# Kernel tuning notes

Hardware: AMD Instinct MI355X
Metric: run time of the kernel (lower is better)

## Reference

```python
import jax, jax.numpy as jnp
import numpy as np

N_NODES = 100000
D = 128
E_ER = 800000
E_EE = 800000
E_RR = 400000


def setup_inputs() -> dict:
    key = jax.random.key(0)
    ks = jax.random.split(key, 16)
    def lin(kw, kb, out_d, in_d):
        s = 1.0 / np.sqrt(in_d)
        w = jax.random.uniform(kw, (out_d, in_d), minval=-s, maxval=s, dtype=jnp.float32)
        b = jax.random.uniform(kb, (out_d,), minval=-s, maxval=s, dtype=jnp.float32)
        return w, b
    W_attn_w, W_attn_b = lin(ks[0], ks[1], D, 2 * D)
    w0_w, w0_b = lin(ks[2], ks[3], 1, D)
    W1_w, W1_b = lin(ks[4], ks[5], D, D)
    W2_w, W2_b = lin(ks[6], ks[7], D, D)
    W3_w, W3_b = lin(ks[8], ks[9], D, D)
    return {
        "node_emb": jax.random.normal(ks[10], (N_NODES, D), dtype=jnp.float32),
        "er_src": jax.random.randint(ks[11], (E_ER,), 0, N_NODES),
        "er_dst": jax.random.randint(ks[12], (E_ER,), 0, N_NODES),
        "ee_src": jax.random.randint(ks[13], (E_EE,), 0, N_NODES),
        "ee_dst": jax.random.randint(ks[14], (E_EE,), 0, N_NODES),
        "ee_weight": jax.random.uniform(ks[15], (E_EE,), dtype=jnp.float32),
        "rr_src": jax.random.randint(jax.random.fold_in(key, 100), (E_RR,), 0, N_NODES),
        "rr_dst": jax.random.randint(jax.random.fold_in(key, 101), (E_RR,), 0, N_NODES),
        "W_attn_w": W_attn_w, "W_attn_b": W_attn_b,
        "w0_w": w0_w, "w0_b": w0_b,
        "W1_w": W1_w, "W1_b": W1_b,
        "W2_w": W2_w, "W2_b": W2_b,
        "W3_w": W3_w, "W3_b": W3_b,
    }


def _segment_softmax(values, segment_ids, num_segments):
    # torch version: seg_max initialized to zeros with include_self=True -> max(0, seg max)
    seg_max = jnp.maximum(jax.ops.segment_max(values, segment_ids, num_segments=num_segments), 0.0)
    exp_v = jnp.exp(values - seg_max[segment_ids])
    seg_sum = jax.ops.segment_sum(exp_v, segment_ids, num_segments=num_segments)
    return exp_v / (seg_sum[segment_ids] + 1e-9)


def reference(node_emb, er_src, er_dst, ee_src, ee_dst, ee_weight, rr_src, rr_dst,
              W_attn_w, W_attn_b, w0_w, w0_b, W1_w, W1_b, W2_w, W2_b, W3_w, W3_b):
    N = node_emb.shape[0]
    # --- attention aggregation over er edges (entity <- relation) ---
    h_emb = node_emb[er_src]            # (E, D)
    r_emb = node_emb[er_dst]            # (E, D)
    pair = jnp.concatenate([r_emb, h_emb], axis=-1)  # (E, 2D)
    e_ij = (jnp.tanh(pair @ W_attn_w.T + W_attn_b) @ w0_w.T + w0_b)[:, 0]  # (E,)
    attn = _segment_softmax(e_ij, er_src, N)
    attn_agg = jax.ops.segment_sum(attn[:, None] * r_emb, er_src, num_segments=N)
    # --- mean aggregation ---
    mean_agg = jax.ops.segment_sum(h_emb, er_dst, num_segments=N)
    mean_cnt = jax.ops.segment_sum(jnp.ones_like(er_dst, dtype=node_emb.dtype), er_dst, num_segments=N)
    w = ee_weight[:, None]
    mean_agg = mean_agg + jax.ops.segment_sum(w * node_emb[ee_dst], ee_src, num_segments=N)
    mean_cnt = mean_cnt + jax.ops.segment_sum(ee_weight, ee_src, num_segments=N)
    mean_agg = mean_agg + jax.ops.segment_sum(node_emb[rr_dst], rr_src, num_segments=N)
    mean_cnt = mean_cnt + jax.ops.segment_sum(jnp.ones_like(rr_src, dtype=node_emb.dtype), rr_src, num_segments=N)
    mean_agg = mean_agg / jnp.clip(mean_cnt, 1.0, None)[:, None]
    return (jnp.tanh(node_emb @ W1_w.T + W1_b)
            + jnp.tanh(attn_agg @ W2_w.T + W2_b)
            + jnp.tanh(mean_agg @ W3_w.T + W3_b))
```

## Files before the change

kernel.cpp:

```cpp
#include <hip/hip_runtime.h>

typedef unsigned int u32;
typedef unsigned short u16;

#define D 128

typedef __attribute__((ext_vector_type(8))) short bf16x8;
typedef __attribute__((ext_vector_type(4))) float f32x4;
#define MFMA16x16(a, b, c) __builtin_amdgcn_mfma_f32_16x16x32_bf16(a, b, c, 0, 0, 0)

__device__ inline float b2f(u32 h) { return __uint_as_float((h & 0xffffu) << 16); }
__device__ inline u16 f2b(float f) {
    u32 u = __float_as_uint(f);
    return (u16)((u + 0x7fffu + ((u >> 16) & 1u)) >> 16);
}
__device__ inline float tanh_fast(float x) {
    x = fminf(fmaxf(x, -15.f), 15.f);
    float e = __expf(2.f * x);
    return (e - 1.f) * __builtin_amdgcn_rcpf(e + 1.f);
}


__global__ __launch_bounds__(256) void k_bhist(const int* __restrict__ er_src,
                                               const int* __restrict__ er_dst,
                                               const int* __restrict__ ee_src,
                                               const int* __restrict__ rr_src,
                                               int* __restrict__ histA,
                                               int* __restrict__ histM,
                                               int E_ER, int E_EE, int E_RR, int NBK) {
    __shared__ int hA[1024], hM[1024];
    int tid = threadIdx.x;
    for (int j = tid; j < NBK; j += 256) { hA[j] = 0; hM[j] = 0; }
    __syncthreads();
    int E_T = 2 * E_ER + E_EE + E_RR;
    int stride = gridDim.x * 256;
    for (int e = blockIdx.x * 256 + tid; e < E_T; e += stride) {
        int i = e;
        if (i < E_ER) { atomicAdd(&hA[er_src[i] >> 7], 1); continue; }
        i -= E_ER;
        int key;
        if (i < E_ER) key = er_dst[i];
        else {
            i -= E_ER;
            key = (i < E_EE) ? ee_src[i] : rr_src[i - E_EE];
        }
        atomicAdd(&hM[key >> 7], 1);
    }
    __syncthreads();
    for (int j = tid; j < NBK; j += 256) {
        histA[j * 256 + blockIdx.x] = hA[j];
        histM[j * 256 + blockIdx.x] = hM[j];
    }
}

__global__ void k_scan1_dual(const int* __restrict__ cnt2, int n,
                             int* __restrict__ off_src, int* __restrict__ off_mean,
                             int* __restrict__ bsum, int nbs) {
    __shared__ int sh[256];
    int b = blockIdx.x;
    const int* cnt = cnt2;
    int* out = off_src;
    int* bs = bsum;
    if (b >= nbs) { b -= nbs; cnt = cnt2 + n; out = off_mean; bs = bsum + 256; }
    int t = threadIdx.x;
    int base = b * 1024 + t * 4;
    int v0 = (base < n) ? cnt[base] : 0;
    int v1 = (base + 1 < n) ? cnt[base + 1] : 0;
    int v2 = (base + 2 < n) ? cnt[base + 2] : 0;
    int v3 = (base + 3 < n) ? cnt[base + 3] : 0;
    int s4 = v0 + v1 + v2 + v3;
    sh[t] = s4;
    __syncthreads();
    for (int o = 1; o < 256; o <<= 1) {
        int x = (t >= o) ? sh[t - o] : 0;
        __syncthreads();
        sh[t] += x;
        __syncthreads();
    }
    int p = sh[t] - s4;
    if (t == 255) bs[b] = sh[255];
    if (base < n) out[base] = p;
    p += v0;
    if (base + 1 < n) out[base + 1] = p;
    p += v1;
    if (base + 2 < n) out[base + 2] = p;
    p += v2;
    if (base + 3 < n) out[base + 3] = p;
}

__global__ void k_scan2_dual(int* __restrict__ bsum, int nb,
                             int* __restrict__ totA, int* __restrict__ totB) {
    __shared__ int sh[256];
    int* bs = bsum + blockIdx.x * 256;
    int* tot = blockIdx.x ? totB : totA;
    int t = threadIdx.x;
    int v = (t < nb) ? bs[t] : 0;
    sh[t] = v;
    __syncthreads();
    for (int o = 1; o < 256; o <<= 1) {
        int x = (t >= o) ? sh[t - o] : 0;
        __syncthreads();
        sh[t] += x;
        __syncthreads();
    }
    if (t < nb) bs[t] = sh[t] - v;
    if (t == 255) *tot = sh[255];
}

__global__ void k_scan3b(int* __restrict__ offA, int* __restrict__ offM,
                         const int* __restrict__ bsum, int n) {
    int i = blockIdx.x * 256 + threadIdx.x;
    if (i < n) offA[i] += bsum[i >> 10];
    else if (i < 2 * n) offM[i - n] += bsum[256 + ((i - n) >> 10)];
}

__global__ __launch_bounds__(256) void k_bin(const int* __restrict__ er_src,
                                             const int* __restrict__ er_dst,
                                             const int* __restrict__ ee_src,
                                             const int* __restrict__ ee_dst,
                                             const int* __restrict__ rr_src,
                                             const int* __restrict__ rr_dst,
                                             const float* __restrict__ ee_w,
                                             const int* __restrict__ offA,
                                             const int* __restrict__ offM,
                                             int* __restrict__ recA,
                                             int2* __restrict__ recM,
                                             int E_ER, int E_EE, int E_RR, int NBK) {
    __shared__ int cA[1024], cM[1024];
    int tid = threadIdx.x, blk = blockIdx.x;
    for (int j = tid; j < NBK; j += 256) {
        cA[j] = offA[j * 256 + blk];
        cM[j] = offM[j * 256 + blk];
    }
    __syncthreads();
    int E_T = 2 * E_ER + E_EE + E_RR;
    int stride = gridDim.x * 256;
    for (int e = blk * 256 + tid; e < E_T; e += stride) {
        int i = e;
        if (i < E_ER) {
            int key = er_src[i];
            int p = atomicAdd(&cA[key >> 7], 1);
            recA[p] = er_dst[i] | ((key & 127) << 17);
            continue;
        }
        i -= E_ER;
        int sct, gat;
        float w;
        if (i < E_ER) {
            sct = er_dst[i]; gat = er_src[i]; w = 1.f;
        } else {
            i -= E_ER;
            if (i < E_EE) { sct = ee_src[i]; gat = ee_dst[i]; w = ee_w[i]; }
            else { i -= E_EE; sct = rr_src[i]; gat = rr_dst[i]; w = 1.f; }
        }
        int p = atomicAdd(&cM[sct >> 7], 1);
        recM[p] = make_int2(gat | ((sct & 127) << 17), __float_as_int(w));
    }
}

__global__ __launch_bounds__(256) void k_bucket(const int* __restrict__ offA_h,
                                                const int* __restrict__ offM_h,
                                                const int* __restrict__ recA,
                                                const int2* __restrict__ recM,
                                                int* __restrict__ off_src,
                                                int* __restrict__ off_mean,
                                                int* __restrict__ er_lst,
                                                int2* __restrict__ gpack,
                                                int E_ER, int E_M, int N, int NBK) {
    __shared__ int cnt[256];
    __shared__ int scanbuf[256];
    __shared__ int cur[256];
    int b = blockIdx.x, tid = threadIdx.x;
    int a0 = offA_h[b * 256];
    int a1 = (b + 1 < NBK) ? offA_h[(b + 1) * 256] : E_ER;
    int m0 = offM_h[b * 256];
    int m1 = (b + 1 < NBK) ? offM_h[(b + 1) * 256] : E_M;
    cnt[tid] = 0;
    __syncthreads();
    for (int i = a0 + tid; i < a1; i += 256) atomicAdd(&cnt[(recA[i] >> 17) & 127], 1);
    for (int i = m0 + tid; i < m1; i += 256) atomicAdd(&cnt[128 + ((recM[i].x >> 17) & 127)], 1);
    __syncthreads();
    int v = cnt[tid];
    scanbuf[tid] = v;
    __syncthreads();
    for (int o = 1; o < 128; o <<= 1) {
        int x = ((tid & 127) >= o) ? scanbuf[tid - o] : 0;
        __syncthreads();
        scanbuf[tid] += x;
        __syncthreads();
    }
    int excl = scanbuf[tid] - v;
    int pos = ((tid < 128) ? a0 : m0) + excl;
    cur[tid] = pos;
    int node = b * 128 + (tid & 127);
    if (node < N) {
        if (tid < 128) off_src[node] = pos;
        else off_mean[node] = pos;
    }
    if (b == 0 && tid == 0) { off_src[N] = E_ER; off_mean[N] = E_M; }
    __syncthreads();
    for (int i = a0 + tid; i < a1; i += 256) {
        int r = recA[i];
        int p = atomicAdd(&cur[(r >> 17) & 127], 1);
        er_lst[p] = r & 0x1FFFF;
    }
    for (int i = m0 + tid; i < m1; i += 256) {
        int2 r = recM[i];
        int p = atomicAdd(&cur[128 + ((r.x >> 17) & 127)], 1);
        gpack[p] = make_int2(r.x & 0x1FFFF, r.y);
    }
}

__global__ void k_cast4(const float* __restrict__ src, u16* __restrict__ dst, int n4) {
    int i = blockIdx.x * 256 + threadIdx.x;
    if (i >= n4) return;
    float4 v = ((const float4*)src)[i];
    ushort4 o;
    o.x = f2b(v.x); o.y = f2b(v.y); o.z = f2b(v.z); o.w = f2b(v.w);
    ((ushort4*)dst)[i] = o;
}

__global__ void k_cast_w(const float* __restrict__ Wattn,
                         const float* __restrict__ W1, const float* __restrict__ W2,
                         const float* __restrict__ W3,
                         u16* __restrict__ Wcat, u16* __restrict__ W123h) {
    int i = blockIdx.x * 256 + threadIdx.x;
    if (i < 32768) {
        int dd = i >> 7, k = i & 127;
        float v = (dd < 128) ? Wattn[(size_t)dd * 256 + k]
                             : Wattn[(size_t)(dd - 128) * 256 + 128 + k];
        Wcat[i] = f2b(v);
        return;
    }
    i -= 32768;
    if (i < 16384) { W123h[i] = f2b(W1[i]); return; }
    i -= 16384;
    if (i < 16384) { W123h[16384 + i] = f2b(W2[i]); return; }
    i -= 16384;
    if (i < 16384) W123h[32768 + i] = f2b(W3[i]);
}

__global__ __launch_bounds__(256) void k_precompute_mfma(const u16* __restrict__ embh,
                                                         const u16* __restrict__ Wcat,
                                                         u16* __restrict__ A, int N) {
    __shared__ u16 sX[64][136];
    int nb = blockIdx.x * 64;
    int tid = threadIdx.x;
    for (int i = tid; i < 1024; i += 256) {
        int row = i >> 4, c8 = i & 15;
        int n = nb + row;
        uint4 v = make_uint4(0u, 0u, 0u, 0u);
        if (n < N) v = *(const uint4*)(embh + (size_t)n * 128 + c8 * 8);
        *(uint4*)&sX[row][c8 * 8] = v;
    }
    __syncthreads();
    int wid = tid >> 6, lane = tid & 63;
    int quad = lane >> 4, l15 = lane & 15;
#pragma unroll
    for (int ns = 0; ns < 4; ns++) {
        int dbase = (wid * 4 + ns) * 16;
        bf16x8 b[4];
#pragma unroll
        for (int ks = 0; ks < 4; ks++)
            b[ks] = *(const bf16x8*)(Wcat + (size_t)(dbase + l15) * 128 + ks * 32 + quad * 8);
#pragma unroll
        for (int ms = 0; ms < 4; ms++) {
            f32x4 acc = {0.f, 0.f, 0.f, 0.f};
#pragma unroll
            for (int ks = 0; ks < 4; ks++) {
                bf16x8 a = *(const bf16x8*)&sX[ms * 16 + l15][ks * 32 + quad * 8];
                acc = MFMA16x16(a, b[ks], acc);
            }
#pragma unroll
            for (int r = 0; r < 4; r++) {
                int row = nb + ms * 16 + quad * 4 + r;
                if (row < N) A[(size_t)row * 256 + dbase + l15] = f2b(acc[r]);
            }
        }
    }
}

__global__ __launch_bounds__(512) void k_fuse(const u16* __restrict__ A,
                                              const int* __restrict__ offA,
                                              const int* __restrict__ lstA,
                                              const int* __restrict__ offM,
                                              const int2* __restrict__ gpack,
                                              const u16* __restrict__ embh,
                                              const float* __restrict__ Wb,
                                              const float* __restrict__ w0w,
                                              const float* __restrict__ w0b,
                                              const u16* __restrict__ W123h,
                                              const float* __restrict__ b1,
                                              const float* __restrict__ b2,
                                              const float* __restrict__ b3,
                                              float* __restrict__ out, int N) {
    __shared__ u16 sX[3][64][136];
    int nb = blockIdx.x * 64;
    int tid = threadIdx.x;
    int wid = tid >> 6, lane = tid & 63;

    for (int j = tid; j < 1024; j += 512) {
        int row = j >> 4, c8 = j & 15;
        int n = nb + row;
        uint4 v = make_uint4(0u, 0u, 0u, 0u);
        if (n < N) v = *(const uint4*)(embh + (size_t)n * 128 + c8 * 8);
        *(uint4*)&sX[0][row][c8 * 8] = v;
    }

    float2 bb = *(const float2*)(Wb + 2 * lane);
    float2 ww = *(const float2*)(w0w + 2 * lane);
    float w0bias = w0b[0];
    for (int i = 0; i < 8; ++i) {
        int local = wid * 8 + i;
        int node = nb + local;
        if (node < N) {
            u32 ah = *(const u32*)(A + (size_t)node * 256 + 128 + 2 * lane);
            float ahx = b2f(ah), ahy = b2f(ah >> 16);
            int s0 = offA[node], s1 = offA[node + 1];
            float l = 0.f, ox = 0.f, oy = 0.f;
            int s = s0;
            for (; s + 2 <= s1; s += 2) {
                int d0 = lstA[s], d1 = lstA[s + 1];
                u32 ar0 = *(const u32*)(A + (size_t)d0 * 256 + 2 * lane);
                u32 ar1 = *(const u32*)(A + (size_t)d1 * 256 + 2 * lane);
                u32 ev0 = *(const u32*)(embh + (size_t)d0 * 128 + 2 * lane);
                u32 ev1 = *(const u32*)(embh + (size_t)d1 * 128 + 2 * lane);
                float p0 = tanh_fast(b2f(ar0) + ahx + bb.x) * ww.x +
                           tanh_fast(b2f(ar0 >> 16) + ahy + bb.y) * ww.y;
                float p1 = tanh_fast(b2f(ar1) + ahx + bb.x) * ww.x +
                           tanh_fast(b2f(ar1 >> 16) + ahy + bb.y) * ww.y;
#pragma unroll
                for (int o = 32; o; o >>= 1) {
                    p0 += __shfl_xor(p0, o);
                    p1 += __shfl_xor(p1, o);
                }
                float e0 = __expf(p0 + w0bias);
                float e1 = __expf(p1 + w0bias);
                l += e0 + e1;
                ox += e0 * b2f(ev0) + e1 * b2f(ev1);
                oy += e0 * b2f(ev0 >> 16) + e1 * b2f(ev1 >> 16);
            }
            if (s < s1) {
                int d0 = lstA[s];
                u32 ar0 = *(const u32*)(A + (size_t)d0 * 256 + 2 * lane);
                u32 ev0 = *(const u32*)(embh + (size_t)d0 * 128 + 2 * lane);
                float p0 = tanh_fast(b2f(ar0) + ahx + bb.x) * ww.x +
                           tanh_fast(b2f(ar0 >> 16) + ahy + bb.y) * ww.y;
#pragma unroll
                for (int o = 32; o; o >>= 1) p0 += __shfl_xor(p0, o);
                float e0 = __expf(p0 + w0bias);
                l += e0;
                ox += e0 * b2f(ev0);
                oy += e0 * b2f(ev0 >> 16);
            }
            float inv = 1.f / (l + 1e-9f);
            *(u32*)&sX[1][local][2 * lane] =
                (u32)f2b(ox * inv) | ((u32)f2b(oy * inv) << 16);

            s0 = offM[node]; s1 = offM[node + 1];
            float ax = 0.f, ay = 0.f, c = 0.f;
            s = s0;
            for (; s + 4 <= s1; s += 4) {
                int2 p0 = gpack[s], p1 = gpack[s + 1], p2 = gpack[s + 2], p3 = gpack[s + 3];
                u32 v0 = *(const u32*)(embh + (size_t)p0.x * 128 + 2 * lane);
                u32 v1 = *(const u32*)(embh + (size_t)p1.x * 128 + 2 * lane);
                u32 v2 = *(const u32*)(embh + (size_t)p2.x * 128 + 2 * lane);
                u32 v3 = *(const u32*)(embh + (size_t)p3.x * 128 + 2 * lane);
                float w0 = __int_as_float(p0.y), w1 = __int_as_float(p1.y);
                float w2 = __int_as_float(p2.y), w3 = __int_as_float(p3.y);
                ax += w0 * b2f(v0) + w1 * b2f(v1) + w2 * b2f(v2) + w3 * b2f(v3);
                ay += w0 * b2f(v0 >> 16) + w1 * b2f(v1 >> 16) +
                      w2 * b2f(v2 >> 16) + w3 * b2f(v3 >> 16);
                c += w0 + w1 + w2 + w3;
            }
            for (; s < s1; ++s) {
                int2 p0 = gpack[s];
                u32 v0 = *(const u32*)(embh + (size_t)p0.x * 128 + 2 * lane);
                float w0 = __int_as_float(p0.y);
                ax += w0 * b2f(v0);
                ay += w0 * b2f(v0 >> 16);
                c += w0;
            }
            c = c > 1.f ? c : 1.f;
            float minv = 1.f / c;
            *(u32*)&sX[2][local][2 * lane] =
                (u32)f2b(ax * minv) | ((u32)f2b(ay * minv) << 16);
        }
    }
    __syncthreads();

    int quad = lane >> 4, l15 = lane & 15;
    int d = wid * 16 + l15;
    const float* biases[3] = {b1, b2, b3};
    f32x4 res0 = {0.f, 0.f, 0.f, 0.f};
    f32x4 res1 = {0.f, 0.f, 0.f, 0.f};
    f32x4 res2 = {0.f, 0.f, 0.f, 0.f};
    f32x4 res3 = {0.f, 0.f, 0.f, 0.f};
#pragma unroll
    for (int arr = 0; arr < 3; arr++) {
        bf16x8 b[4];
#pragma unroll
        for (int ks = 0; ks < 4; ks++)
            b[ks] = *(const bf16x8*)(W123h + (size_t)arr * 16384 +
                                     (size_t)d * 128 + ks * 32 + quad * 8);
        float bias = biases[arr][d];
#pragma unroll
        for (int ms = 0; ms < 4; ms++) {
            f32x4 acc = {0.f, 0.f, 0.f, 0.f};
#pragma unroll
            for (int ks = 0; ks < 4; ks++) {
                bf16x8 a = *(const bf16x8*)&sX[arr][ms * 16 + l15][ks * 32 + quad * 8];
                acc = MFMA16x16(a, b[ks], acc);
            }
            f32x4& res = (ms == 0) ? res0 : (ms == 1) ? res1 : (ms == 2) ? res2 : res3;
#pragma unroll
            for (int r = 0; r < 4; r++)
                res[r] += tanh_fast(acc[r] + bias);
        }
    }
#pragma unroll
    for (int ms = 0; ms < 4; ms++) {
        f32x4& res = (ms == 0) ? res0 : (ms == 1) ? res1 : (ms == 2) ? res2 : res3;
#pragma unroll
        for (int r = 0; r < 4; r++) {
            int orow = nb + ms * 16 + quad * 4 + r;
            if (orow < N)
                out[(size_t)orow * 128 + d] = res[r];
        }
    }
}

extern "C" void kernel_launch(void* const* d_in, const int* in_sizes, int n_in,
                              void* d_out, int out_size, void* d_ws, size_t ws_size,
                              hipStream_t stream) {
    const float* emb     = (const float*)d_in[0];
    const int*   er_src  = (const int*)d_in[1];
    const int*   er_dst  = (const int*)d_in[2];
    const int*   ee_src  = (const int*)d_in[3];
    const int*   ee_dst  = (const int*)d_in[4];
    const float* ee_w    = (const float*)d_in[5];
    const int*   rr_src  = (const int*)d_in[6];
    const int*   rr_dst  = (const int*)d_in[7];
    const float* Wattn   = (const float*)d_in[8];
    const float* Wattn_b = (const float*)d_in[9];
    const float* w0w     = (const float*)d_in[10];
    const float* w0b     = (const float*)d_in[11];
    const float* W1      = (const float*)d_in[12];
    const float* b1      = (const float*)d_in[13];
    const float* W2      = (const float*)d_in[14];
    const float* b2      = (const float*)d_in[15];
    const float* W3      = (const float*)d_in[16];
    const float* b3      = (const float*)d_in[17];
    float* out = (float*)d_out;

    int N    = in_sizes[0] / D;
    int E_ER = in_sizes[1];
    int E_EE = in_sizes[3];
    int E_RR = in_sizes[6];
    int E_M  = E_ER + E_EE + E_RR;

    int NBK = (N + 127) >> 7;
    int HL  = NBK * 256;

    char* ws = (char*)d_ws;
    size_t off_b = 0;
    auto alloc = [&](size_t bytes) -> void* {
        void* p = ws + off_b;
        off_b += (bytes + 255) & ~(size_t)255;
        return p;
    };
    u16*   embh   = (u16*)alloc((size_t)N * 128 * 2);
    u16*   A      = (u16*)alloc((size_t)N * 256 * 2);
    u16*   Wcat_h = (u16*)alloc(256 * 128 * 2);
    u16*   W123h  = (u16*)alloc(3 * 128 * 128 * 2);
    int*   off_src  = (int*)alloc((size_t)(N + 1) * 4);
    int*   off_mean = (int*)alloc((size_t)(N + 1) * 4);
    int*   bsum     = (int*)alloc(514 * 4);
    int*   er_lst   = (int*)alloc((size_t)E_ER * 4);
    int2*  gpack    = (int2*)alloc((size_t)E_M * 8);

    char* Ab   = (char*)A;
    int2* recM = (int2*)Ab;
    int*  recA = (int*)(Ab + (size_t)E_M * 8);
    int*  hist2 = (int*)(Ab + (size_t)E_M * 8 + (size_t)E_ER * 4);
    int*  offHA = hist2 + 2 * HL;
    int*  offHM = offHA + HL;

    int nbh = (HL + 1023) / 1024;

    k_cast4<<<((N * 128 / 4) + 255) / 256, 256, 0, stream>>>(emb, embh, N * 128 / 4);
    k_cast_w<<<(81920 + 255) / 256, 256, 0, stream>>>(Wattn, W1, W2, W3, Wcat_h, W123h);

    k_bhist<<<256, 256, 0, stream>>>(er_src, er_dst, ee_src, rr_src,
                                     hist2, hist2 + HL, E_ER, E_EE, E_RR, NBK);
    k_scan1_dual<<<2 * nbh, 256, 0, stream>>>(hist2, HL, offHA, offHM, bsum, nbh);
    k_scan2_dual<<<2, 256, 0, stream>>>(bsum, nbh, bsum + 512, bsum + 513);
    k_scan3b<<<(2 * HL + 255) / 256, 256, 0, stream>>>(offHA, offHM, bsum, HL);
    k_bin<<<256, 256, 0, stream>>>(er_src, er_dst, ee_src, ee_dst, rr_src, rr_dst, ee_w,
                                   offHA, offHM, recA, recM, E_ER, E_EE, E_RR, NBK);
    k_bucket<<<NBK, 256, 0, stream>>>(offHA, offHM, recA, recM,
                                      off_src, off_mean, er_lst, gpack,
                                      E_ER, E_M, N, NBK);

    k_precompute_mfma<<<(N + 63) / 64, 256, 0, stream>>>(embh, Wcat_h, A, N);
    k_fuse<<<(N + 63) / 64, 512, 0, stream>>>(A, off_src, er_lst, off_mean, gpack,
                                              embh, Wattn_b, w0w, w0b, W123h,
                                              b1, b2, b3, out, N);
}
```

Before: 533.0 us.

## Interleave projections and bf16 embeddings into one row buffer for gather locality

Packs the attention projection halves and the bf16 node embedding into a single 384-element row per node, so an edge gather reads the projection and the embedding from one contiguous row. The attention edge loop is unrolled from 2 to 4 edges to put more gathers in flight, and the bias add is hoisted out of it. The fuse kernel now reads self-embedding MFMA operands straight from global memory instead of staging them in shared memory, which cuts LDS use by a third. In exchange, temporary buffers that used to alias the projection buffer get their own workspace allocations, and the direct global operand loads may cost more than LDS reads.

```diff
diff --git a/kernel.cpp b/kernel.cpp
--- a/kernel.cpp
+++ b/kernel.cpp
@@ -19,6 +19,8 @@
     float e = __expf(2.f * x);
     return (e - 1.f) * __builtin_amdgcn_rcpf(e + 1.f);
 }
+
+#define PROW 384
 
 
 __global__ __launch_bounds__(256) void k_bhist(const int* __restrict__ er_src,
@@ -211,13 +213,15 @@
     }
 }
 
-__global__ void k_cast4(const float* __restrict__ src, u16* __restrict__ dst, int n4) {
+__global__ void k_cast4(const float* __restrict__ src, u16* __restrict__ P, int n4) {
     int i = blockIdx.x * 256 + threadIdx.x;
     if (i >= n4) return;
     float4 v = ((const float4*)src)[i];
     ushort4 o;
     o.x = f2b(v.x); o.y = f2b(v.y); o.z = f2b(v.z); o.w = f2b(v.w);
-    ((ushort4*)dst)[i] = o;
+    int base = i * 4;
+    int n = base >> 7, d = base & 127;
+    *(ushort4*)(P + (size_t)n * PROW + 128 + d) = o;
 }
 
 __global__ void k_cast_w(const float* __restrict__ Wattn,
@@ -240,9 +244,8 @@
     if (i < 16384) W123h[32768 + i] = f2b(W3[i]);
 }
 
-__global__ __launch_bounds__(256) void k_precompute_mfma(const u16* __restrict__ embh,
-                                                         const u16* __restrict__ Wcat,
-                                                         u16* __restrict__ A, int N) {
+__global__ __launch_bounds__(256) void k_precompute_mfma(const u16* __restrict__ Wcat,
+                                                         u16* __restrict__ P, int N) {
     __shared__ u16 sX[64][136];
     int nb = blockIdx.x * 64;
     int tid = threadIdx.x;
@@ -250,7 +253,7 @@
         int row = i >> 4, c8 = i & 15;
         int n = nb + row;
         uint4 v = make_uint4(0u, 0u, 0u, 0u);
-        if (n < N) v = *(const uint4*)(embh + (size_t)n * 128 + c8 * 8);
+        if (n < N) v = *(const uint4*)(P + (size_t)n * PROW + 128 + c8 * 8);
         *(uint4*)&sX[row][c8 * 8] = v;
     }
     __syncthreads();
@@ -259,6 +262,7 @@
 #pragma unroll
     for (int ns = 0; ns < 4; ns++) {
         int dbase = (wid * 4 + ns) * 16;
+        int cbase = dbase + (dbase >= 128 ? 128 : 0);
         bf16x8 b[4];
 #pragma unroll
         for (int ks = 0; ks < 4; ks++)
@@ -274,18 +278,17 @@
 #pragma unroll
             for (int r = 0; r < 4; r++) {
                 int row = nb + ms * 16 + quad * 4 + r;
-                if (row < N) A[(size_t)row * 256 + dbase + l15] = f2b(acc[r]);
-            }
-        }
-    }
-}
-
-__global__ __launch_bounds__(512) void k_fuse(const u16* __restrict__ A,
+                if (row < N) P[(size_t)row * PROW + cbase + l15] = f2b(acc[r]);
+            }
+        }
+    }
+}
+
+__global__ __launch_bounds__(512) void k_fuse(const u16* __restrict__ P,
                                               const int* __restrict__ offA,
                                               const int* __restrict__ lstA,
                                               const int* __restrict__ offM,
                                               const int2* __restrict__ gpack,
-                                              const u16* __restrict__ embh,
                                               const float* __restrict__ Wb,
                                               const float* __restrict__ w0w,
                                               const float* __restrict__ w0b,
@@ -294,58 +297,64 @@
                                               const float* __restrict__ b2,
                                               const float* __restrict__ b3,
                                               float* __restrict__ out, int N) {
-    __shared__ u16 sX[3][64][136];
+    __shared__ u16 sX[2][64][136];
     int nb = blockIdx.x * 64;
     int tid = threadIdx.x;
     int wid = tid >> 6, lane = tid & 63;
 
-    for (int j = tid; j < 1024; j += 512) {
-        int row = j >> 4, c8 = j & 15;
-        int n = nb + row;
-        uint4 v = make_uint4(0u, 0u, 0u, 0u);
-        if (n < N) v = *(const uint4*)(embh + (size_t)n * 128 + c8 * 8);
-        *(uint4*)&sX[0][row][c8 * 8] = v;
-    }
-
     float2 bb = *(const float2*)(Wb + 2 * lane);
     float2 ww = *(const float2*)(w0w + 2 * lane);
     float w0bias = w0b[0];
+
     for (int i = 0; i < 8; ++i) {
         int local = wid * 8 + i;
         int node = nb + local;
         if (node < N) {
-            u32 ah = *(const u32*)(A + (size_t)node * 256 + 128 + 2 * lane);
-            float ahx = b2f(ah), ahy = b2f(ah >> 16);
+            u32 ah = *(const u32*)(P + (size_t)node * PROW + 256 + 2 * lane);
+            float axb = b2f(ah) + bb.x, ayb = b2f(ah >> 16) + bb.y;
             int s0 = offA[node], s1 = offA[node + 1];
             float l = 0.f, ox = 0.f, oy = 0.f;
             int s = s0;
-            for (; s + 2 <= s1; s += 2) {
-                int d0 = lstA[s], d1 = lstA[s + 1];
-                u32 ar0 = *(const u32*)(A + (size_t)d0 * 256 + 2 * lane);
-                u32 ar1 = *(const u32*)(A + (size_t)d1 * 256 + 2 * lane);
-                u32 ev0 = *(const u32*)(embh + (size_t)d0 * 128 + 2 * lane);
-                u32 ev1 = *(const u32*)(embh + (size_t)d1 * 128 + 2 * lane);
-                float p0 = tanh_fast(b2f(ar0) + ahx + bb.x) * ww.x +
-                           tanh_fast(b2f(ar0 >> 16) + ahy + bb.y) * ww.y;
-                float p1 = tanh_fast(b2f(ar1) + ahx + bb.x) * ww.x +
-                           tanh_fast(b2f(ar1 >> 16) + ahy + bb.y) * ww.y;
+            for (; s + 4 <= s1; s += 4) {
+                int d0 = lstA[s], d1 = lstA[s + 1], d2 = lstA[s + 2], d3 = lstA[s + 3];
+                const u16* r0 = P + (size_t)d0 * PROW;
+                const u16* r1 = P + (size_t)d1 * PROW;
+                const u16* r2 = P + (size_t)d2 * PROW;
+                const u16* r3 = P + (size_t)d3 * PROW;
+                u32 ar0 = *(const u32*)(r0 + 2 * lane);
+                u32 ar1 = *(const u32*)(r1 + 2 * lane);
+                u32 ar2 = *(const u32*)(r2 + 2 * lane);
+                u32 ar3 = *(const u32*)(r3 + 2 * lane);
+                u32 ev0 = *(const u32*)(r0 + 128 + 2 * lane);
+                u32 ev1 = *(const u32*)(r1 + 128 + 2 * lane);
+                u32 ev2 = *(const u32*)(r2 + 128 + 2 * lane);
+                u32 ev3 = *(const u32*)(r3 + 128 + 2 * lane);
+                float p0 = tanh_fast(b2f(ar0) + axb) * ww.x + tanh_fast(b2f(ar0 >> 16) + ayb) * ww.y;
+                float p1 = tanh_fast(b2f(ar1) + axb) * ww.x + tanh_fast(b2f(ar1 >> 16) + ayb) * ww.y;
+                float p2 = tanh_fast(b2f(ar2) + axb) * ww.x + tanh_fast(b2f(ar2 >> 16) + ayb) * ww.y;
+                float p3 = tanh_fast(b2f(ar3) + axb) * ww.x + tanh_fast(b2f(ar3 >> 16) + ayb) * ww.y;
 #pragma unroll
                 for (int o = 32; o; o >>= 1) {
                     p0 += __shfl_xor(p0, o);
                     p1 += __shfl_xor(p1, o);
+                    p2 += __shfl_xor(p2, o);
+                    p3 += __shfl_xor(p3, o);
                 }
                 float e0 = __expf(p0 + w0bias);
                 float e1 = __expf(p1 + w0bias);
-                l += e0 + e1;
-                ox += e0 * b2f(ev0) + e1 * b2f(ev1);
-                oy += e0 * b2f(ev0 >> 16) + e1 * b2f(ev1 >> 16);
-            }
-            if (s < s1) {
+                float e2 = __expf(p2 + w0bias);
+                float e3 = __expf(p3 + w0bias);
+                l += (e0 + e1) + (e2 + e3);
+                ox += e0 * b2f(ev0) + e1 * b2f(ev1) + e2 * b2f(ev2) + e3 * b2f(ev3);
+                oy += e0 * b2f(ev0 >> 16) + e1 * b2f(ev1 >> 16) +
+                      e2 * b2f(ev2 >> 16) + e3 * b2f(ev3 >> 16);
+            }
+            for (; s < s1; ++s) {
                 int d0 = lstA[s];
-                u32 ar0 = *(const u32*)(A + (size_t)d0 * 256 + 2 * lane);
-                u32 ev0 = *(const u32*)(embh + (size_t)d0 * 128 + 2 * lane);
-                float p0 = tanh_fast(b2f(ar0) + ahx + bb.x) * ww.x +
-                           tanh_fast(b2f(ar0 >> 16) + ahy + bb.y) * ww.y;
+                const u16* r0 = P + (size_t)d0 * PROW;
+                u32 ar0 = *(const u32*)(r0 + 2 * lane);
+                u32 ev0 = *(const u32*)(r0 + 128 + 2 * lane);
+                float p0 = tanh_fast(b2f(ar0) + axb) * ww.x + tanh_fast(b2f(ar0 >> 16) + ayb) * ww.y;
 #pragma unroll
                 for (int o = 32; o; o >>= 1) p0 += __shfl_xor(p0, o);
                 float e0 = __expf(p0 + w0bias);
@@ -354,7 +363,7 @@
                 oy += e0 * b2f(ev0 >> 16);
             }
             float inv = 1.f / (l + 1e-9f);
-            *(u32*)&sX[1][local][2 * lane] =
+            *(u32*)&sX[0][local][2 * lane] =
                 (u32)f2b(ox * inv) | ((u32)f2b(oy * inv) << 16);
 
             s0 = offM[node]; s1 = offM[node + 1];
@@ -362,10 +371,10 @@
             s = s0;
             for (; s + 4 <= s1; s += 4) {
                 int2 p0 = gpack[s], p1 = gpack[s + 1], p2 = gpack[s + 2], p3 = gpack[s + 3];
-                u32 v0 = *(const u32*)(embh + (size_t)p0.x * 128 + 2 * lane);
-                u32 v1 = *(const u32*)(embh + (size_t)p1.x * 128 + 2 * lane);
-                u32 v2 = *(const u32*)(embh + (size_t)p2.x * 128 + 2 * lane);
-                u32 v3 = *(const u32*)(embh + (size_t)p3.x * 128 + 2 * lane);
+                u32 v0 = *(const u32*)(P + (size_t)p0.x * PROW + 128 + 2 * lane);
+                u32 v1 = *(const u32*)(P + (size_t)p1.x * PROW + 128 + 2 * lane);
+                u32 v2 = *(const u32*)(P + (size_t)p2.x * PROW + 128 + 2 * lane);
+                u32 v3 = *(const u32*)(P + (size_t)p3.x * PROW + 128 + 2 * lane);
                 float w0 = __int_as_float(p0.y), w1 = __int_as_float(p1.y);
                 float w2 = __int_as_float(p2.y), w3 = __int_as_float(p3.y);
                 ax += w0 * b2f(v0) + w1 * b2f(v1) + w2 * b2f(v2) + w3 * b2f(v3);
@@ -375,7 +384,7 @@
             }
             for (; s < s1; ++s) {
                 int2 p0 = gpack[s];
-                u32 v0 = *(const u32*)(embh + (size_t)p0.x * 128 + 2 * lane);
+                u32 v0 = *(const u32*)(P + (size_t)p0.x * PROW + 128 + 2 * lane);
                 float w0 = __int_as_float(p0.y);
                 ax += w0 * b2f(v0);
                 ay += w0 * b2f(v0 >> 16);
@@ -383,7 +392,7 @@
             }
             c = c > 1.f ? c : 1.f;
             float minv = 1.f / c;
-            *(u32*)&sX[2][local][2 * lane] =
+            *(u32*)&sX[1][local][2 * lane] =
                 (u32)f2b(ax * minv) | ((u32)f2b(ay * minv) << 16);
         }
     }
@@ -406,10 +415,14 @@
         float bias = biases[arr][d];
 #pragma unroll
         for (int ms = 0; ms < 4; ms++) {
+            int row = nb + ms * 16 + l15;
+            int rc = row < N ? row : N - 1;
             f32x4 acc = {0.f, 0.f, 0.f, 0.f};
 #pragma unroll
             for (int ks = 0; ks < 4; ks++) {
-                bf16x8 a = *(const bf16x8*)&sX[arr][ms * 16 + l15][ks * 32 + quad * 8];
+                bf16x8 a = (arr == 0)
+                    ? *(const bf16x8*)(P + (size_t)rc * PROW + 128 + ks * 32 + quad * 8)
+                    : *(const bf16x8*)&sX[arr - 1][ms * 16 + l15][ks * 32 + quad * 8];
                 acc = MFMA16x16(a, b[ks], acc);
             }
             f32x4& res = (ms == 0) ? res0 : (ms == 1) ? res1 : (ms == 2) ? res2 : res3;
@@ -469,8 +482,7 @@
         off_b += (bytes + 255) & ~(size_t)255;
         return p;
     };
-    u16*   embh   = (u16*)alloc((size_t)N * 128 * 2);
-    u16*   A      = (u16*)alloc((size_t)N * 256 * 2);
+    u16*   P      = (u16*)alloc((size_t)N * PROW * 2);
     u16*   Wcat_h = (u16*)alloc(256 * 128 * 2);
     u16*   W123h  = (u16*)alloc(3 * 128 * 128 * 2);
     int*   off_src  = (int*)alloc((size_t)(N + 1) * 4);
@@ -478,17 +490,15 @@
     int*   bsum     = (int*)alloc(514 * 4);
     int*   er_lst   = (int*)alloc((size_t)E_ER * 4);
     int2*  gpack    = (int2*)alloc((size_t)E_M * 8);
-
-    char* Ab   = (char*)A;
-    int2* recM = (int2*)Ab;
-    int*  recA = (int*)(Ab + (size_t)E_M * 8);
-    int*  hist2 = (int*)(Ab + (size_t)E_M * 8 + (size_t)E_ER * 4);
-    int*  offHA = hist2 + 2 * HL;
-    int*  offHM = offHA + HL;
+    int2*  recM     = (int2*)alloc((size_t)E_M * 8);
+    int*   recA     = (int*)alloc((size_t)E_ER * 4);
+    int*   hist2    = (int*)alloc((size_t)2 * HL * 4);
+    int*   offHA    = (int*)alloc((size_t)HL * 4);
+    int*   offHM    = (int*)alloc((size_t)HL * 4);
 
     int nbh = (HL + 1023) / 1024;
 
-    k_cast4<<<((N * 128 / 4) + 255) / 256, 256, 0, stream>>>(emb, embh, N * 128 / 4);
+    k_cast4<<<((N * 128 / 4) + 255) / 256, 256, 0, stream>>>(emb, P, N * 128 / 4);
     k_cast_w<<<(81920 + 255) / 256, 256, 0, stream>>>(Wattn, W1, W2, W3, Wcat_h, W123h);
 
     k_bhist<<<256, 256, 0, stream>>>(er_src, er_dst, ee_src, rr_src,
@@ -502,8 +512,8 @@
                                       off_src, off_mean, er_lst, gpack,
                                       E_ER, E_M, N, NBK);
 
-    k_precompute_mfma<<<(N + 63) / 64, 256, 0, stream>>>(embh, Wcat_h, A, N);
-    k_fuse<<<(N + 63) / 64, 512, 0, stream>>>(A, off_src, er_lst, off_mean, gpack,
-                                              embh, Wattn_b, w0w, w0b, W123h,
+    k_precompute_mfma<<<(N + 63) / 64, 256, 0, stream>>>(Wcat_h, P, N);
+    k_fuse<<<(N + 63) / 64, 512, 0, stream>>>(P, off_src, er_lst, off_mean, gpack,
+                                              Wattn_b, w0w, w0b, W123h,
                                               b1, b2, b3, out, N);
 }
```

Result: slower. 592.5 us (+11.2%).

## Process four edges per wavefront with 16-byte row loads in gather loops

Applied to the files above, without the earlier changes.

The per-node gather loops are reorganised so that each 16-lane quarter of a wavefront handles a different edge. Each lane loads 8 bf16 values with one 16-byte load instead of 2 values per lane, so a wave now processes up to 8 edges per iteration rather than 2 or 4. Partial sums are combined across quarters with cross-lane shuffles at the end. The aim is fewer, wider memory requests and more memory-level parallelism per wave. The cost is wasted lanes on low-degree nodes (tail masking) and extra shuffle reductions.

```diff
diff --git a/kernel.cpp b/kernel.cpp
--- a/kernel.cpp
+++ b/kernel.cpp
@@ -298,6 +298,7 @@
     int nb = blockIdx.x * 64;
     int tid = threadIdx.x;
     int wid = tid >> 6, lane = tid & 63;
+    int quad = lane >> 4, l15 = lane & 15;
 
     for (int j = tid; j < 1024; j += 512) {
         int row = j >> 4, c8 = j & 15;
@@ -307,89 +308,125 @@
         *(uint4*)&sX[0][row][c8 * 8] = v;
     }
 
-    float2 bb = *(const float2*)(Wb + 2 * lane);
-    float2 ww = *(const float2*)(w0w + 2 * lane);
+    float wwv[8], bbv[8];
+#pragma unroll
+    for (int j = 0; j < 8; j++) {
+        wwv[j] = w0w[l15 * 8 + j];
+        bbv[j] = Wb[l15 * 8 + j];
+    }
     float w0bias = w0b[0];
+
     for (int i = 0; i < 8; ++i) {
         int local = wid * 8 + i;
         int node = nb + local;
         if (node < N) {
-            u32 ah = *(const u32*)(A + (size_t)node * 256 + 128 + 2 * lane);
-            float ahx = b2f(ah), ahy = b2f(ah >> 16);
+            bf16x8 ah8 = *(const bf16x8*)(A + (size_t)node * 256 + 128 + l15 * 8);
+            const u32* ahp = (const u32*)&ah8;
+            float haxb[8];
+#pragma unroll
+            for (int j = 0; j < 4; j++) {
+                haxb[2 * j]     = b2f(ahp[j]) + bbv[2 * j];
+                haxb[2 * j + 1] = b2f(ahp[j] >> 16) + bbv[2 * j + 1];
+            }
             int s0 = offA[node], s1 = offA[node + 1];
-            float l = 0.f, ox = 0.f, oy = 0.f;
-            int s = s0;
-            for (; s + 2 <= s1; s += 2) {
-                int d0 = lstA[s], d1 = lstA[s + 1];
-                u32 ar0 = *(const u32*)(A + (size_t)d0 * 256 + 2 * lane);
-                u32 ar1 = *(const u32*)(A + (size_t)d1 * 256 + 2 * lane);
-                u32 ev0 = *(const u32*)(embh + (size_t)d0 * 128 + 2 * lane);
-                u32 ev1 = *(const u32*)(embh + (size_t)d1 * 128 + 2 * lane);
-                float p0 = tanh_fast(b2f(ar0) + ahx + bb.x) * ww.x +
-                           tanh_fast(b2f(ar0 >> 16) + ahy + bb.y) * ww.y;
-                float p1 = tanh_fast(b2f(ar1) + ahx + bb.x) * ww.x +
-                           tanh_fast(b2f(ar1 >> 16) + ahy + bb.y) * ww.y;
-#pragma unroll
-                for (int o = 32; o; o >>= 1) {
+            float accx[8] = {0.f, 0.f, 0.f, 0.f, 0.f, 0.f, 0.f, 0.f};
+            float lsum = 0.f;
+            for (int s = s0; s < s1; s += 8) {
+                int i0 = s + quad, i1 = s + 4 + quad;
+                bool va = i0 < s1, vb = i1 < s1;
+                int d0 = lstA[va ? i0 : s0];
+                int d1 = lstA[vb ? i1 : s0];
+                bf16x8 ar0 = *(const bf16x8*)(A + (size_t)d0 * 256 + l15 * 8);
+                bf16x8 ar1 = *(const bf16x8*)(A + (size_t)d1 * 256 + l15 * 8);
+                bf16x8 ev0 = *(const bf16x8*)(embh + (size_t)d0 * 128 + l15 * 8);
+                bf16x8 ev1 = *(const bf16x8*)(embh + (size_t)d1 * 128 + l15 * 8);
+                const u32* a0p = (const u32*)&ar0;
+                const u32* a1p = (const u32*)&ar1;
+                float p0 = 0.f, p1 = 0.f;
+#pragma unroll
+                for (int j = 0; j < 4; j++) {
+                    p0 += tanh_fast(b2f(a0p[j]) + haxb[2 * j]) * wwv[2 * j] +
+                          tanh_fast(b2f(a0p[j] >> 16) + haxb[2 * j + 1]) * wwv[2 * j + 1];
+                    p1 += tanh_fast(b2f(a1p[j]) + haxb[2 * j]) * wwv[2 * j] +
+                          tanh_fast(b2f(a1p[j] >> 16) + haxb[2 * j + 1]) * wwv[2 * j + 1];
+                }
+#pragma unroll
+                for (int o = 1; o < 16; o <<= 1) {
                     p0 += __shfl_xor(p0, o);
                     p1 += __shfl_xor(p1, o);
                 }
-                float e0 = __expf(p0 + w0bias);
-                float e1 = __expf(p1 + w0bias);
-                l += e0 + e1;
-                ox += e0 * b2f(ev0) + e1 * b2f(ev1);
-                oy += e0 * b2f(ev0 >> 16) + e1 * b2f(ev1 >> 16);
-            }
-            if (s < s1) {
-                int d0 = lstA[s];
-                u32 ar0 = *(const u32*)(A + (size_t)d0 * 256 + 2 * lane);
-                u32 ev0 = *(const u32*)(embh + (size_t)d0 * 128 + 2 * lane);
-                float p0 = tanh_fast(b2f(ar0) + ahx + bb.x) * ww.x +
-                           tanh_fast(b2f(ar0 >> 16) + ahy + bb.y) * ww.y;
-#pragma unroll
-                for (int o = 32; o; o >>= 1) p0 += __shfl_xor(p0, o);
-                float e0 = __expf(p0 + w0bias);
-                l += e0;
-                ox += e0 * b2f(ev0);
-                oy += e0 * b2f(ev0 >> 16);
-            }
-            float inv = 1.f / (l + 1e-9f);
-            *(u32*)&sX[1][local][2 * lane] =
-                (u32)f2b(ox * inv) | ((u32)f2b(oy * inv) << 16);
+                float e0 = va ? __expf(p0 + w0bias) : 0.f;
+                float e1 = vb ? __expf(p1 + w0bias) : 0.f;
+                lsum += e0 + e1;
+                const u32* e0p = (const u32*)&ev0;
+                const u32* e1p = (const u32*)&ev1;
+#pragma unroll
+                for (int j = 0; j < 4; j++) {
+                    accx[2 * j]     += e0 * b2f(e0p[j]) + e1 * b2f(e1p[j]);
+                    accx[2 * j + 1] += e0 * b2f(e0p[j] >> 16) + e1 * b2f(e1p[j] >> 16);
+                }
+            }
+#pragma unroll
+            for (int j = 0; j < 8; j++) {
+                accx[j] += __shfl_xor(accx[j], 16);
+                accx[j] += __shfl_xor(accx[j], 32);
+            }
+            lsum += __shfl_xor(lsum, 16);
+            lsum += __shfl_xor(lsum, 32);
+            float inv = 1.f / (lsum + 1e-9f);
+            if (quad == 0) {
+                uint4 o4;
+                u32* op = (u32*)&o4;
+#pragma unroll
+                for (int j = 0; j < 4; j++)
+                    op[j] = (u32)f2b(accx[2 * j] * inv) |
+                            ((u32)f2b(accx[2 * j + 1] * inv) << 16);
+                *(uint4*)&sX[1][local][l15 * 8] = o4;
+            }
 
             s0 = offM[node]; s1 = offM[node + 1];
-            float ax = 0.f, ay = 0.f, c = 0.f;
-            s = s0;
-            for (; s + 4 <= s1; s += 4) {
-                int2 p0 = gpack[s], p1 = gpack[s + 1], p2 = gpack[s + 2], p3 = gpack[s + 3];
-                u32 v0 = *(const u32*)(embh + (size_t)p0.x * 128 + 2 * lane);
-                u32 v1 = *(const u32*)(embh + (size_t)p1.x * 128 + 2 * lane);
-                u32 v2 = *(const u32*)(embh + (size_t)p2.x * 128 + 2 * lane);
-                u32 v3 = *(const u32*)(embh + (size_t)p3.x * 128 + 2 * lane);
-                float w0 = __int_as_float(p0.y), w1 = __int_as_float(p1.y);
-                float w2 = __int_as_float(p2.y), w3 = __int_as_float(p3.y);
-                ax += w0 * b2f(v0) + w1 * b2f(v1) + w2 * b2f(v2) + w3 * b2f(v3);
-                ay += w0 * b2f(v0 >> 16) + w1 * b2f(v1 >> 16) +
-                      w2 * b2f(v2 >> 16) + w3 * b2f(v3 >> 16);
-                c += w0 + w1 + w2 + w3;
-            }
-            for (; s < s1; ++s) {
-                int2 p0 = gpack[s];
-                u32 v0 = *(const u32*)(embh + (size_t)p0.x * 128 + 2 * lane);
-                float w0 = __int_as_float(p0.y);
-                ax += w0 * b2f(v0);
-                ay += w0 * b2f(v0 >> 16);
-                c += w0;
-            }
+            float accm[8] = {0.f, 0.f, 0.f, 0.f, 0.f, 0.f, 0.f, 0.f};
+            float c = 0.f;
+            for (int s = s0; s < s1; s += 8) {
+                int i0 = s + quad, i1 = s + 4 + quad;
+                bool va = i0 < s1, vb = i1 < s1;
+                int2 pk0 = gpack[va ? i0 : s0];
+                int2 pk1 = gpack[vb ? i1 : s0];
+                float w0 = va ? __int_as_float(pk0.y) : 0.f;
+                float w1 = vb ? __int_as_float(pk1.y) : 0.f;
+                bf16x8 ev0 = *(const bf16x8*)(embh + (size_t)pk0.x * 128 + l15 * 8);
+                bf16x8 ev1 = *(const bf16x8*)(embh + (size_t)pk1.x * 128 + l15 * 8);
+                const u32* e0p = (const u32*)&ev0;
+                const u32* e1p = (const u32*)&ev1;
+#pragma unroll
+                for (int j = 0; j < 4; j++) {
+                    accm[2 * j]     += w0 * b2f(e0p[j]) + w1 * b2f(e1p[j]);
+                    accm[2 * j + 1] += w0 * b2f(e0p[j] >> 16) + w1 * b2f(e1p[j] >> 16);
+                }
+                c += w0 + w1;
+            }
+#pragma unroll
+            for (int j = 0; j < 8; j++) {
+                accm[j] += __shfl_xor(accm[j], 16);
+                accm[j] += __shfl_xor(accm[j], 32);
+            }
+            c += __shfl_xor(c, 16);
+            c += __shfl_xor(c, 32);
             c = c > 1.f ? c : 1.f;
             float minv = 1.f / c;
-            *(u32*)&sX[2][local][2 * lane] =
-                (u32)f2b(ax * minv) | ((u32)f2b(ay * minv) << 16);
-        }
-    }
-    __syncthreads();
-
-    int quad = lane >> 4, l15 = lane & 15;
+            if (quad == 0) {
+                uint4 o4;
+                u32* op = (u32*)&o4;
+#pragma unroll
+                for (int j = 0; j < 4; j++)
+                    op[j] = (u32)f2b(accm[2 * j] * minv) |
+                            ((u32)f2b(accm[2 * j + 1] * minv) << 16);
+                *(uint4*)&sX[2][local][l15 * 8] = o4;
+            }
+        }
+    }
+    __syncthreads();
+
     int d = wid * 16 + l15;
     const float* biases[3] = {b1, b2, b3};
     f32x4 res0 = {0.f, 0.f, 0.f, 0.f};
```

Measured after the change: 508.6 us (median of 2 runs). 4.6% less time.
